# Optimization experiments

Measured on AMD Instinct MI355X. Metric: run time of the kernel, lower is better.

The kernel has to match this reference:

```python
import jax, jax.numpy as jnp
import numpy as np

T = 8192        # timesteps
IN = 512        # input_size
H = 1024        # hidden_layer_size
OUT = 256       # output_size
STEP = 0.25     # ODE solver step_size
NSUB = 4        # euler substeps per unit time interval (t spacing = 1)


def setup_inputs() -> dict:
    key = jax.random.key(0)
    ks = jax.random.split(key, 16)
    def lin(k, out_d, in_d):
        kw, kb = jax.random.split(k)
        W = jax.random.normal(kw, (out_d, in_d), jnp.float32) / np.sqrt(in_d).astype(np.float32)
        b = jax.random.normal(kb, (out_d, 1), jnp.float32) * 0.01
        return W, b
    W_in, b_in = lin(ks[0], H, IN)      # linear_in
    W_h, b_h = lin(ks[1], H, H)         # linear_hidden
    W_h2, b_h2 = lin(ks[2], H, H)       # linear_hidden2
    W_f1, b_f1 = lin(ks[3], H, H)       # ode_func.linear
    W_f2, b_f2 = lin(ks[4], H, H)       # ode_func.linear2
    W_dec, b_dec = lin(ks[5], OUT, H)   # decoder
    x = jax.random.normal(ks[6], (T, IN, 1), jnp.float32)
    t = jnp.arange(T, dtype=jnp.float32)
    return dict(t=t, x=x, W_in=W_in, b_in=b_in, W_h=W_h, b_h=b_h,
                W_h2=W_h2, b_h2=b_h2, W_f1=W_f1, b_f1=b_f1,
                W_f2=W_f2, b_f2=b_f2, W_dec=W_dec, b_dec=b_dec)


def reference(t, x, W_in, b_in, W_h, b_h, W_h2, b_h2, W_f1, b_f1, W_f2, b_f2, W_dec, b_dec):
    # ODE_Func: f(h) = W_f2 @ tanh(W_f1 @ h + b_f1) + b_f2   (autonomous; t unused)
    def ode_f(h):
        return W_f2 @ jnp.tanh(W_f1 @ h + b_f1) + b_f2

    dts = (t[1:] - t[:-1]) / NSUB  # (T-1,) euler substep sizes (fixed-grid euler)

    def step(h, inp):
        x_i, dt = inp
        # odeint(ode_func, h, t[i-1:i+1], method='euler', step_size=STEP)
        for _ in range(NSUB):
            h = h + dt * ode_f(h)
        # RNN cell update
        pre = W_in @ x_i + b_in + W_h @ h + b_h          # (H,1)
        h_new = jnp.tanh(W_h2 @ jnp.tanh(pre) + b_h2)    # (H,1)
        return h_new, None

    h0 = jnp.zeros((W_h.shape[0], 1), x.dtype)
    # original loop skips i == 0 entirely (h stays zeros there)
    h_T, _ = jax.lax.scan(step, h0, (x[1:], dts))
    return W_dec @ h_T + b_dec  # (OUT, 1)
```

## Files before the change

kernel.cpp:

```cpp
#include <hip/hip_runtime.h>
#include <math.h>


#define TSTEPS 8192
#define INP    512
#define HDIM   1024
#define OUTD   256
#define NWG    64
#define BLK    256

typedef unsigned long long u64;
typedef unsigned int u32;

__device__ __forceinline__ u64 aload(u64* p) {
    return __hip_atomic_load(p, __ATOMIC_RELAXED, __HIP_MEMORY_SCOPE_AGENT);
}
__device__ __forceinline__ void astore(u64* p, u64 v) {
    __hip_atomic_store(p, v, __ATOMIC_RELAXED, __HIP_MEMORY_SCOPE_AGENT);
}
__device__ __forceinline__ u64 pack(u32 tag, float f) {
    return ((u64)tag << 32) | (u64)__float_as_uint(f);
}

__global__ __launch_bounds__(256)
void mm1024(const float* __restrict__ A, const float* __restrict__ B,
            float* __restrict__ C) {
    __shared__ float As[64][17];
    __shared__ float Bs[16][65];
    const int tid = threadIdx.x;
    const int tx = tid & 15, ty = tid >> 4;
    const int r0 = blockIdx.y * 64, c0 = blockIdx.x * 64;
    float acc[4][4] = {};
    for (int k0 = 0; k0 < HDIM; k0 += 16) {
        const int ar = tid >> 2, ac = (tid & 3) * 4;
        const float4 av = *reinterpret_cast<const float4*>(
            A + (size_t)(r0 + ar) * HDIM + k0 + ac);
        As[ar][ac] = av.x; As[ar][ac + 1] = av.y;
        As[ar][ac + 2] = av.z; As[ar][ac + 3] = av.w;
        const int br = tid >> 4, bc = (tid & 15) * 4;
        const float4 bv = *reinterpret_cast<const float4*>(
            B + (size_t)(k0 + br) * HDIM + c0 + bc);
        Bs[br][bc] = bv.x; Bs[br][bc + 1] = bv.y;
        Bs[br][bc + 2] = bv.z; Bs[br][bc + 3] = bv.w;
        __syncthreads();
        #pragma unroll
        for (int kk = 0; kk < 16; ++kk) {
            float a[4], b[4];
            #pragma unroll
            for (int i2 = 0; i2 < 4; ++i2) a[i2] = As[ty * 4 + i2][kk];
            #pragma unroll
            for (int j2 = 0; j2 < 4; ++j2) b[j2] = Bs[kk][tx * 4 + j2];
            #pragma unroll
            for (int i2 = 0; i2 < 4; ++i2)
                #pragma unroll
                for (int j2 = 0; j2 < 4; ++j2)
                    acc[i2][j2] = fmaf(a[i2], b[j2], acc[i2][j2]);
        }
        __syncthreads();
    }
    #pragma unroll
    for (int i2 = 0; i2 < 4; ++i2)
        #pragma unroll
        for (int j2 = 0; j2 < 4; ++j2)
            C[(size_t)(r0 + ty * 4 + i2) * HDIM + c0 + tx * 4 + j2] = acc[i2][j2];
}

__global__ __launch_bounds__(BLK, 1)
void ode_rnn_persistent(
    const float* __restrict__ t,    const float* __restrict__ x,
    const float* __restrict__ W_in, const float* __restrict__ b_in,
    const float* __restrict__ W_h,  const float* __restrict__ b_h,
    const float* __restrict__ W_h2, const float* __restrict__ b_h2,
    const float* __restrict__ W_f1, const float* __restrict__ b_f1,
    const float* __restrict__ b_f2,
    const float* __restrict__ W_dec, const float* __restrict__ b_dec,
    const float* __restrict__ Mw,   const float* __restrict__ Pw,
    float* __restrict__ out,
    u64* QA, u64* QB, u64* QC, u64* QD)
{
    __shared__ __align__(16) float lds[HDIM];
    const int tid = threadIdx.x;
    const int wg  = blockIdx.x;
    const int seg = tid & 15;
    const int row = wg * 16 + (tid >> 4);

    auto stage = [&](u64* q, u32 tag) {
        __syncthreads();
        const int i0 = tid, i1 = tid + 256, i2 = tid + 512, i3 = tid + 768;
        u64 v0, v1, v2, v3;
        for (;;) {
            v0 = aload(q + i0); v1 = aload(q + i1);
            v2 = aload(q + i2); v3 = aload(q + i3);
            const bool ok = ((u32)(v0 >> 32) == tag) & ((u32)(v1 >> 32) == tag) &
                            ((u32)(v2 >> 32) == tag) & ((u32)(v3 >> 32) == tag);
            if (ok) break;
        }
        lds[i0] = __uint_as_float((u32)v0); lds[i1] = __uint_as_float((u32)v1);
        lds[i2] = __uint_as_float((u32)v2); lds[i3] = __uint_as_float((u32)v3);
        __syncthreads();
    };

    auto pref16 = [&](float4* w, const float* Wbase) {
        const float4* p = reinterpret_cast<const float4*>(Wbase + (size_t)row * HDIM);
        #pragma unroll
        for (int j = 0; j < 16; ++j) w[j] = p[j * 16 + seg];
    };
    auto dot16 = [&](const float4* w) {
        float a = 0.f;
        #pragma unroll
        for (int j = 0; j < 16; ++j) {
            const float4 v = *reinterpret_cast<const float4*>(lds + j * 64 + seg * 4);
            a = fmaf(w[j].x, v.x, a); a = fmaf(w[j].y, v.y, a);
            a = fmaf(w[j].z, v.z, a); a = fmaf(w[j].w, v.w, a);
        }
        return a;
    };
    auto reduce16 = [&](float a) {
        #pragma unroll
        for (int off = 8; off; off >>= 1) a += __shfl_down(a, off, 16);
        return a;
    };

    const float bf1_r = b_f1[row];
    const float bih_r = b_in[row] + b_h[row];
    const float bh2_r = b_h2[row];

    float c1_own, c2_own;
    {
        #pragma unroll
        for (int k = 0; k < 4; ++k) lds[tid + k * 256] = b_f2[tid + k * 256];
        __syncthreads();
        float4 w[16];
        pref16(w, W_f1); c1_own = reduce16(dot16(w));
        pref16(w, W_h);  c2_own = reduce16(dot16(w));
    }

    float z_own = bf1_r;
    float y_own = 0.f;
    u32 eA = 0, eB = 0, eC = 0, eD = 0;
    float4 wa[16], wb[16];

    #pragma unroll 1
    for (int i = 1; i < TSTEPS; ++i) {
        const float dt = (t[i] - t[i - 1]) * 0.25f;

        ++eA;
        if (seg == 0) astore(&QA[row], pack(eA, tanhf(z_own)));
        float4 xr[8], wir[8];
        {
            const float4* xp = reinterpret_cast<const float4*>(x + (size_t)i * INP);
            const float4* wp = reinterpret_cast<const float4*>(W_in + (size_t)row * INP);
            #pragma unroll
            for (int j = 0; j < 8; ++j) { xr[j] = xp[j * 16 + seg]; wir[j] = wp[j * 16 + seg]; }
        }
        pref16(wa, Mw); pref16(wb, Pw);
        stage(QA, eA);
        float winx;
        {
            float a_ = 0.f;
            #pragma unroll
            for (int j = 0; j < 8; ++j) {
                a_ = fmaf(wir[j].x, xr[j].x, a_); a_ = fmaf(wir[j].y, xr[j].y, a_);
                a_ = fmaf(wir[j].z, xr[j].z, a_); a_ = fmaf(wir[j].w, xr[j].w, a_);
            }
            winx = reduce16(a_);
        }
        {
            const float md = reduce16(dot16(wa));
            const float pd = reduce16(dot16(wb));
            if (seg == 0) { z_own = fmaf(dt, md + c1_own, z_own);
                            y_own = fmaf(dt, pd + c2_own, y_own); }
        }

        ++eB;
        if (seg == 0) astore(&QB[row], pack(eB, tanhf(z_own)));
        pref16(wa, Mw); pref16(wb, Pw);
        stage(QB, eB);
        {
            const float md = reduce16(dot16(wa));
            const float pd = reduce16(dot16(wb));
            if (seg == 0) { z_own = fmaf(dt, md + c1_own, z_own);
                            y_own = fmaf(dt, pd + c2_own, y_own); }
        }

        ++eA;
        if (seg == 0) astore(&QA[row], pack(eA, tanhf(z_own)));
        pref16(wa, Mw); pref16(wb, Pw);
        stage(QA, eA);
        {
            const float md = reduce16(dot16(wa));
            const float pd = reduce16(dot16(wb));
            if (seg == 0) { z_own = fmaf(dt, md + c1_own, z_own);
                            y_own = fmaf(dt, pd + c2_own, y_own); }
        }

        ++eB;
        if (seg == 0) astore(&QB[row], pack(eB, tanhf(z_own)));
        pref16(wb, Pw);
        stage(QB, eB);
        float a_val = 0.f;
        {
            const float pd = reduce16(dot16(wb));
            if (seg == 0) {
                const float y4 = fmaf(dt, pd + c2_own, y_own);
                a_val = tanhf(y4 + winx + bih_r);
            }
        }

        ++eC;
        if (seg == 0) astore(&QC[row], pack(eC, a_val));
        pref16(wa, W_h2);
        stage(QC, eC);
        float h_new = 0.f;
        {
            const float hd = reduce16(dot16(wa));
            if (seg == 0) h_new = tanhf(hd + bh2_r);
        }

        ++eD;
        if (seg == 0) astore(&QD[row], pack(eD, h_new));
        pref16(wa, W_f1);
        stage(QD, eD);
        {
            const float zd = reduce16(dot16(wa));
            pref16(wb, W_h);
            const float yd = reduce16(dot16(wb));
            if (seg == 0) { z_own = zd + bf1_r; y_own = yd; }
        }
    }

    {
        const int rl = tid >> 6, s2 = tid & 63;
        const int orow = wg * 4 + rl;
        const float4* wd = reinterpret_cast<const float4*>(W_dec + (size_t)orow * HDIM);
        float acc = 0.f;
        #pragma unroll
        for (int j = 0; j < 4; ++j) {
            const float4 w = wd[j * 64 + s2];
            const float4 v = *reinterpret_cast<const float4*>(lds + j * 256 + s2 * 4);
            acc = fmaf(w.x, v.x, acc); acc = fmaf(w.y, v.y, acc);
            acc = fmaf(w.z, v.z, acc); acc = fmaf(w.w, v.w, acc);
        }
        #pragma unroll
        for (int off = 32; off; off >>= 1) acc += __shfl_down(acc, off, 64);
        if (s2 == 0) out[orow] = acc + b_dec[orow];
    }
}

extern "C" void kernel_launch(void* const* d_in, const int* in_sizes, int n_in,
                              void* d_out, int out_size, void* d_ws, size_t ws_size,
                              hipStream_t stream) {
    const float* t     = (const float*)d_in[0];
    const float* x     = (const float*)d_in[1];
    const float* W_in  = (const float*)d_in[2];
    const float* b_in  = (const float*)d_in[3];
    const float* W_h   = (const float*)d_in[4];
    const float* b_h   = (const float*)d_in[5];
    const float* W_h2  = (const float*)d_in[6];
    const float* b_h2  = (const float*)d_in[7];
    const float* W_f1  = (const float*)d_in[8];
    const float* b_f1  = (const float*)d_in[9];
    const float* W_f2  = (const float*)d_in[10];
    const float* b_f2  = (const float*)d_in[11];
    const float* W_dec = (const float*)d_in[12];
    const float* b_dec = (const float*)d_in[13];
    float* out = (float*)d_out;

    unsigned char* ws = (unsigned char*)d_ws;
    float* Mw = (float*)(ws);
    float* Pw = (float*)(ws + (size_t)4 * 1024 * 1024);
    u64*   QA = (u64*)(ws + (size_t)8 * 1024 * 1024);
    u64*   QB = QA + HDIM;
    u64*   QC = QB + HDIM;
    u64*   QD = QC + HDIM;

    mm1024<<<dim3(16, 16), 256, 0, stream>>>(W_f1, W_f2, Mw);
    mm1024<<<dim3(16, 16), 256, 0, stream>>>(W_h,  W_f2, Pw);

    hipMemsetAsync(ws + (size_t)8 * 1024 * 1024, 0, 4 * HDIM * sizeof(u64), stream);

    ode_rnn_persistent<<<dim3(NWG), dim3(BLK), 0, stream>>>(
        t, x, W_in, b_in, W_h, b_h, W_h2, b_h2, W_f1, b_f1, b_f2,
        W_dec, b_dec, Mw, Pw, out, QA, QB, QC, QD);
}
```

Baseline: 100.5 ms.

## Restructure persistent ODE-RNN to 256 single-wave blocks with register-resident weights

Splits the persistent kernel from 64 blocks of 256 threads into 256 single-wavefront blocks that each own 4 hidden rows. The M and P operator rows and the W_in rows are now kept in registers for the whole run instead of being reloaded every substep. Each wave polls the flag-tagged exchange queues directly into registers and uses wave-wide shuffle reductions, which removes the LDS staging and __syncthreads barriers. The cost is much higher register pressure and more blocks spinning on the global queues at every stage.

After: 123.5 ms. 22.9% more time.

```diff
diff --git a/kernel.cpp b/kernel.cpp
--- a/kernel.cpp
+++ b/kernel.cpp
@@ -6,8 +6,8 @@
 #define INP    512
 #define HDIM   1024
 #define OUTD   256
-#define NWG    64
-#define BLK    256
+#define NWG    256
+#define BLK    64
 
 typedef unsigned long long u64;
 typedef unsigned int u32;
@@ -78,172 +78,210 @@
     float* __restrict__ out,
     u64* QA, u64* QB, u64* QC, u64* QD)
 {
-    __shared__ __align__(16) float lds[HDIM];
-    const int tid = threadIdx.x;
-    const int wg  = blockIdx.x;
-    const int seg = tid & 15;
-    const int row = wg * 16 + (tid >> 4);
-
-    auto stage = [&](u64* q, u32 tag) {
-        __syncthreads();
-        const int i0 = tid, i1 = tid + 256, i2 = tid + 512, i3 = tid + 768;
-        u64 v0, v1, v2, v3;
+    const int lane = threadIdx.x;
+    const int gw   = blockIdx.x;
+    const int r0   = gw * 4;
+
+    auto bflyAll = [&](float& a) {
+        #pragma unroll
+        for (int off = 32; off; off >>= 1) a += __shfl_xor(a, off);
+    };
+    auto sel4 = [&](const float (&a)[4]) {
+        float s = a[0];
+        s = (lane == 1) ? a[1] : s;
+        s = (lane == 2) ? a[2] : s;
+        s = (lane == 3) ? a[3] : s;
+        return s;
+    };
+    auto pubTanh = [&](u64* q, u32 e, float pre) {
+        if (lane < 4) astore(&q[r0 + lane], pack(e, tanhf(pre)));
+    };
+    auto waitq = [&](u64* q, u32 tag, u64 (&v)[16]) {
         for (;;) {
-            v0 = aload(q + i0); v1 = aload(q + i1);
-            v2 = aload(q + i2); v3 = aload(q + i3);
-            const bool ok = ((u32)(v0 >> 32) == tag) & ((u32)(v1 >> 32) == tag) &
-                            ((u32)(v2 >> 32) == tag) & ((u32)(v3 >> 32) == tag);
-            if (ok) break;
-        }
-        lds[i0] = __uint_as_float((u32)v0); lds[i1] = __uint_as_float((u32)v1);
-        lds[i2] = __uint_as_float((u32)v2); lds[i3] = __uint_as_float((u32)v3);
-        __syncthreads();
-    };
-
-    auto pref16 = [&](float4* w, const float* Wbase) {
-        const float4* p = reinterpret_cast<const float4*>(Wbase + (size_t)row * HDIM);
-        #pragma unroll
-        for (int j = 0; j < 16; ++j) w[j] = p[j * 16 + seg];
-    };
-    auto dot16 = [&](const float4* w) {
-        float a = 0.f;
+            #pragma unroll
+            for (int j = 0; j < 16; ++j) v[j] = aload(q + j * 64 + lane);
+            bool ok = true;
+            #pragma unroll
+            for (int j = 0; j < 16; ++j) ok &= ((u32)(v[j] >> 32) == tag);
+            if (__all(ok)) break;
+        }
+    };
+    auto loadRows16 = [&](const float* __restrict__ W, float (&w)[4][16]) {
+        #pragma unroll
+        for (int r = 0; r < 4; ++r)
+            #pragma unroll
+            for (int j = 0; j < 16; ++j)
+                w[r][j] = W[(size_t)(r0 + r) * HDIM + j * 64 + lane];
+    };
+    auto dotDual = [&](const float (&wa)[4][16], const float (&wb)[4][16],
+                       const u64 (&v)[16], float (&oa)[4], float (&ob)[4]) {
+        float aa[4] = {}, ab[4] = {};
         #pragma unroll
         for (int j = 0; j < 16; ++j) {
-            const float4 v = *reinterpret_cast<const float4*>(lds + j * 64 + seg * 4);
-            a = fmaf(w[j].x, v.x, a); a = fmaf(w[j].y, v.y, a);
-            a = fmaf(w[j].z, v.z, a); a = fmaf(w[j].w, v.w, a);
-        }
-        return a;
-    };
-    auto reduce16 = [&](float a) {
-        #pragma unroll
-        for (int off = 8; off; off >>= 1) a += __shfl_down(a, off, 16);
-        return a;
-    };
-
-    const float bf1_r = b_f1[row];
-    const float bih_r = b_in[row] + b_h[row];
-    const float bh2_r = b_h2[row];
-
-    float c1_own, c2_own;
+            const float uv = __uint_as_float((u32)v[j]);
+            #pragma unroll
+            for (int r = 0; r < 4; ++r) {
+                aa[r] = fmaf(wa[r][j], uv, aa[r]);
+                ab[r] = fmaf(wb[r][j], uv, ab[r]);
+            }
+        }
+        #pragma unroll
+        for (int off = 32; off; off >>= 1)
+            #pragma unroll
+            for (int r = 0; r < 4; ++r) {
+                aa[r] += __shfl_xor(aa[r], off);
+                ab[r] += __shfl_xor(ab[r], off);
+            }
+        #pragma unroll
+        for (int r = 0; r < 4; ++r) { oa[r] = aa[r]; ob[r] = ab[r]; }
+    };
+    auto dotOne = [&](const float (&wa)[4][16], const u64 (&v)[16],
+                      float (&oa)[4]) {
+        float aa[4] = {};
+        #pragma unroll
+        for (int j = 0; j < 16; ++j) {
+            const float uv = __uint_as_float((u32)v[j]);
+            #pragma unroll
+            for (int r = 0; r < 4; ++r) aa[r] = fmaf(wa[r][j], uv, aa[r]);
+        }
+        #pragma unroll
+        for (int off = 32; off; off >>= 1)
+            #pragma unroll
+            for (int r = 0; r < 4; ++r) aa[r] += __shfl_xor(aa[r], off);
+        #pragma unroll
+        for (int r = 0; r < 4; ++r) oa[r] = aa[r];
+    };
+
+    float m[4][16], p[4][16];
+    loadRows16(Mw, m);
+    loadRows16(Pw, p);
+    float wir[4][8];
+    #pragma unroll
+    for (int r = 0; r < 4; ++r)
+        #pragma unroll
+        for (int j = 0; j < 8; ++j)
+            wir[r][j] = W_in[(size_t)(r0 + r) * INP + j * 64 + lane];
+
+    float bf1r[4], bihr[4], bh2r[4];
+    #pragma unroll
+    for (int r = 0; r < 4; ++r) {
+        bf1r[r] = b_f1[r0 + r];
+        bihr[r] = b_in[r0 + r] + b_h[r0 + r];
+        bh2r[r] = b_h2[r0 + r];
+    }
+
+    float c1[4], c2[4];
     {
-        #pragma unroll
-        for (int k = 0; k < 4; ++k) lds[tid + k * 256] = b_f2[tid + k * 256];
-        __syncthreads();
-        float4 w[16];
-        pref16(w, W_f1); c1_own = reduce16(dot16(w));
-        pref16(w, W_h);  c2_own = reduce16(dot16(w));
-    }
-
-    float z_own = bf1_r;
-    float y_own = 0.f;
+        float bv[16];
+        #pragma unroll
+        for (int j = 0; j < 16; ++j) bv[j] = b_f2[j * 64 + lane];
+        float wt[4][16];
+        loadRows16(W_f1, wt);
+        #pragma unroll
+        for (int r = 0; r < 4; ++r) {
+            float a = 0.f;
+            #pragma unroll
+            for (int j = 0; j < 16; ++j) a = fmaf(wt[r][j], bv[j], a);
+            bflyAll(a); c1[r] = a;
+        }
+        loadRows16(W_h, wt);
+        #pragma unroll
+        for (int r = 0; r < 4; ++r) {
+            float a = 0.f;
+            #pragma unroll
+            for (int j = 0; j < 16; ++j) a = fmaf(wt[r][j], bv[j], a);
+            bflyAll(a); c2[r] = a;
+        }
+    }
+
+    float z[4], y[4];
+    #pragma unroll
+    for (int r = 0; r < 4; ++r) { z[r] = bf1r[r]; y[r] = 0.f; }
+
     u32 eA = 0, eB = 0, eC = 0, eD = 0;
-    float4 wa[16], wb[16];
+    u64 v[16];
+    float xr[8];
+    float wbufA[4][16], wbufB[4][16];
+
+    auto odeSub = [&](u64* q, u32 e, float dt) {
+        pubTanh(q, e, sel4(z));
+        waitq(q, e, v);
+        float md[4], pd[4];
+        dotDual(m, p, v, md, pd);
+        #pragma unroll
+        for (int r = 0; r < 4; ++r) {
+            z[r] = fmaf(dt, md[r] + c1[r], z[r]);
+            y[r] = fmaf(dt, pd[r] + c2[r], y[r]);
+        }
+    };
 
     #pragma unroll 1
     for (int i = 1; i < TSTEPS; ++i) {
         const float dt = (t[i] - t[i - 1]) * 0.25f;
-
-        ++eA;
-        if (seg == 0) astore(&QA[row], pack(eA, tanhf(z_own)));
-        float4 xr[8], wir[8];
+        const float* xrow = x + (size_t)i * INP;
+
+        odeSub(QA, ++eA, dt);
+        #pragma unroll
+        for (int j = 0; j < 8; ++j) xr[j] = xrow[j * 64 + lane];
+        odeSub(QB, ++eB, dt);
+        odeSub(QA, ++eA, dt);
+
+        ++eB;
+        pubTanh(QB, eB, sel4(z));
+        float winx[4];
         {
-            const float4* xp = reinterpret_cast<const float4*>(x + (size_t)i * INP);
-            const float4* wp = reinterpret_cast<const float4*>(W_in + (size_t)row * INP);
-            #pragma unroll
-            for (int j = 0; j < 8; ++j) { xr[j] = xp[j * 16 + seg]; wir[j] = wp[j * 16 + seg]; }
-        }
-        pref16(wa, Mw); pref16(wb, Pw);
-        stage(QA, eA);
-        float winx;
-        {
-            float a_ = 0.f;
-            #pragma unroll
-            for (int j = 0; j < 8; ++j) {
-                a_ = fmaf(wir[j].x, xr[j].x, a_); a_ = fmaf(wir[j].y, xr[j].y, a_);
-                a_ = fmaf(wir[j].z, xr[j].z, a_); a_ = fmaf(wir[j].w, xr[j].w, a_);
-            }
-            winx = reduce16(a_);
-        }
-        {
-            const float md = reduce16(dot16(wa));
-            const float pd = reduce16(dot16(wb));
-            if (seg == 0) { z_own = fmaf(dt, md + c1_own, z_own);
-                            y_own = fmaf(dt, pd + c2_own, y_own); }
-        }
-
-        ++eB;
-        if (seg == 0) astore(&QB[row], pack(eB, tanhf(z_own)));
-        pref16(wa, Mw); pref16(wb, Pw);
-        stage(QB, eB);
-        {
-            const float md = reduce16(dot16(wa));
-            const float pd = reduce16(dot16(wb));
-            if (seg == 0) { z_own = fmaf(dt, md + c1_own, z_own);
-                            y_own = fmaf(dt, pd + c2_own, y_own); }
-        }
-
-        ++eA;
-        if (seg == 0) astore(&QA[row], pack(eA, tanhf(z_own)));
-        pref16(wa, Mw); pref16(wb, Pw);
-        stage(QA, eA);
-        {
-            const float md = reduce16(dot16(wa));
-            const float pd = reduce16(dot16(wb));
-            if (seg == 0) { z_own = fmaf(dt, md + c1_own, z_own);
-                            y_own = fmaf(dt, pd + c2_own, y_own); }
-        }
-
-        ++eB;
-        if (seg == 0) astore(&QB[row], pack(eB, tanhf(z_own)));
-        pref16(wb, Pw);
-        stage(QB, eB);
-        float a_val = 0.f;
-        {
-            const float pd = reduce16(dot16(wb));
-            if (seg == 0) {
-                const float y4 = fmaf(dt, pd + c2_own, y_own);
-                a_val = tanhf(y4 + winx + bih_r);
-            }
-        }
+            float aw[4] = {};
+            #pragma unroll
+            for (int j = 0; j < 8; ++j)
+                #pragma unroll
+                for (int r = 0; r < 4; ++r)
+                    aw[r] = fmaf(wir[r][j], xr[j], aw[r]);
+            #pragma unroll
+            for (int off = 32; off; off >>= 1)
+                #pragma unroll
+                for (int r = 0; r < 4; ++r) aw[r] += __shfl_xor(aw[r], off);
+            #pragma unroll
+            for (int r = 0; r < 4; ++r) winx[r] = aw[r];
+        }
+        waitq(QB, eB, v);
+        float pd[4];
+        dotOne(p, v, pd);
+        float apre[4];
+        #pragma unroll
+        for (int r = 0; r < 4; ++r)
+            apre[r] = fmaf(dt, pd[r] + c2[r], y[r]) + winx[r] + bihr[r];
 
         ++eC;
-        if (seg == 0) astore(&QC[row], pack(eC, a_val));
-        pref16(wa, W_h2);
-        stage(QC, eC);
-        float h_new = 0.f;
-        {
-            const float hd = reduce16(dot16(wa));
-            if (seg == 0) h_new = tanhf(hd + bh2_r);
-        }
+        pubTanh(QC, eC, sel4(apre));
+        loadRows16(W_h2, wbufA);
+        waitq(QC, eC, v);
+        float hd[4];
+        dotOne(wbufA, v, hd);
+        float hpre[4];
+        #pragma unroll
+        for (int r = 0; r < 4; ++r) hpre[r] = hd[r] + bh2r[r];
 
         ++eD;
-        if (seg == 0) astore(&QD[row], pack(eD, h_new));
-        pref16(wa, W_f1);
-        stage(QD, eD);
-        {
-            const float zd = reduce16(dot16(wa));
-            pref16(wb, W_h);
-            const float yd = reduce16(dot16(wb));
-            if (seg == 0) { z_own = zd + bf1_r; y_own = yd; }
-        }
-    }
-
+        pubTanh(QD, eD, sel4(hpre));
+        loadRows16(W_f1, wbufA);
+        loadRows16(W_h, wbufB);
+        waitq(QD, eD, v);
+        float zd[4], yd[4];
+        dotDual(wbufA, wbufB, v, zd, yd);
+        #pragma unroll
+        for (int r = 0; r < 4; ++r) { z[r] = zd[r] + bf1r[r]; y[r] = yd[r]; }
+    }
+
+    waitq(QD, eD, v);
     {
-        const int rl = tid >> 6, s2 = tid & 63;
-        const int orow = wg * 4 + rl;
-        const float4* wd = reinterpret_cast<const float4*>(W_dec + (size_t)orow * HDIM);
         float acc = 0.f;
         #pragma unroll
-        for (int j = 0; j < 4; ++j) {
-            const float4 w = wd[j * 64 + s2];
-            const float4 v = *reinterpret_cast<const float4*>(lds + j * 256 + s2 * 4);
-            acc = fmaf(w.x, v.x, acc); acc = fmaf(w.y, v.y, acc);
-            acc = fmaf(w.z, v.z, acc); acc = fmaf(w.w, v.w, acc);
-        }
-        #pragma unroll
-        for (int off = 32; off; off >>= 1) acc += __shfl_down(acc, off, 64);
-        if (s2 == 0) out[orow] = acc + b_dec[orow];
+        for (int j = 0; j < 16; ++j) {
+            const float w = W_dec[(size_t)gw * HDIM + j * 64 + lane];
+            acc = fmaf(w, __uint_as_float((u32)v[j]), acc);
+        }
+        bflyAll(acc);
+        if (lane == 0) out[gw] = acc + b_dec[gw];
     }
 }
 
```

## Keep Mw/Pw/W_in rows register-resident and replicate exchange queues across WGs

Applied to the files above, without the earlier changes.

Mw, Pw and W_in rows are now loaded into registers once before the time loop instead of being refetched from memory at every Euler substep. The inter-workgroup exchange buffers are replicated eight times; each workgroup publishes to all replicas and polls the one chosen by its block index, which spreads out the polling traffic. Tanh is moved from the producer into publish, dot products are fused in pairs sharing the LDS reads, and W_h2/W_f1/W_h loads are reordered to overlap with waits. This raises register pressure to roughly 80 float4 per thread and multiplies the publish stores by eight.

New measurement: 105.3 ms. 1.05x slower.

```diff
diff --git a/kernel.cpp b/kernel.cpp
--- a/kernel.cpp
+++ b/kernel.cpp
@@ -8,6 +8,7 @@
 #define OUTD   256
 #define NWG    64
 #define BLK    256
+#define NREP   8
 
 typedef unsigned long long u64;
 typedef unsigned int u32;
@@ -83,14 +84,20 @@
     const int wg  = blockIdx.x;
     const int seg = tid & 15;
     const int row = wg * 16 + (tid >> 4);
+    const int rep = wg & (NREP - 1);
+
+    auto publish = [&](u64* q, u32 e, float pre) {
+        if (seg < 8) astore(q + (size_t)seg * HDIM + row, pack(e, tanhf(pre)));
+    };
 
     auto stage = [&](u64* q, u32 tag) {
+        u64* base = q + (size_t)rep * HDIM;
         __syncthreads();
         const int i0 = tid, i1 = tid + 256, i2 = tid + 512, i3 = tid + 768;
         u64 v0, v1, v2, v3;
         for (;;) {
-            v0 = aload(q + i0); v1 = aload(q + i1);
-            v2 = aload(q + i2); v3 = aload(q + i3);
+            v0 = aload(base + i0); v1 = aload(base + i1);
+            v2 = aload(base + i2); v3 = aload(base + i3);
             const bool ok = ((u32)(v0 >> 32) == tag) & ((u32)(v1 >> 32) == tag) &
                             ((u32)(v2 >> 32) == tag) & ((u32)(v3 >> 32) == tag);
             if (ok) break;
@@ -100,12 +107,17 @@
         __syncthreads();
     };
 
-    auto pref16 = [&](float4* w, const float* Wbase) {
-        const float4* p = reinterpret_cast<const float4*>(Wbase + (size_t)row * HDIM);
-        #pragma unroll
-        for (int j = 0; j < 16; ++j) w[j] = p[j * 16 + seg];
-    };
-    auto dot16 = [&](const float4* w) {
+    auto pref16 = [&](const float* W, float4 (&w)[16]) {
+        const float4* pW = reinterpret_cast<const float4*>(W + (size_t)row * HDIM);
+        #pragma unroll
+        for (int j = 0; j < 16; ++j) w[j] = pW[j * 16 + seg];
+    };
+    auto red16 = [&](float a) {
+        #pragma unroll
+        for (int off = 8; off; off >>= 1) a += __shfl_xor(a, off, 16);
+        return a;
+    };
+    auto dotLds = [&](const float4 (&w)[16]) {
         float a = 0.f;
         #pragma unroll
         for (int j = 0; j < 16; ++j) {
@@ -113,119 +125,121 @@
             a = fmaf(w[j].x, v.x, a); a = fmaf(w[j].y, v.y, a);
             a = fmaf(w[j].z, v.z, a); a = fmaf(w[j].w, v.w, a);
         }
-        return a;
-    };
-    auto reduce16 = [&](float a) {
-        #pragma unroll
-        for (int off = 8; off; off >>= 1) a += __shfl_down(a, off, 16);
-        return a;
-    };
+        return red16(a);
+    };
+    auto dotLds2 = [&](const float4 (&wa)[16], const float4 (&wb)[16],
+                       float& oa, float& ob) {
+        float a = 0.f, b = 0.f;
+        #pragma unroll
+        for (int j = 0; j < 16; ++j) {
+            const float4 v = *reinterpret_cast<const float4*>(lds + j * 64 + seg * 4);
+            a = fmaf(wa[j].x, v.x, a); a = fmaf(wa[j].y, v.y, a);
+            a = fmaf(wa[j].z, v.z, a); a = fmaf(wa[j].w, v.w, a);
+            b = fmaf(wb[j].x, v.x, b); b = fmaf(wb[j].y, v.y, b);
+            b = fmaf(wb[j].z, v.z, b); b = fmaf(wb[j].w, v.w, b);
+        }
+        oa = red16(a); ob = red16(b);
+    };
+
+    float4 m16[16], p16[16], wir[8];
+    pref16(Mw, m16);
+    pref16(Pw, p16);
+    {
+        const float4* pW = reinterpret_cast<const float4*>(W_in + (size_t)row * INP);
+        #pragma unroll
+        for (int j = 0; j < 8; ++j) wir[j] = pW[j * 16 + seg];
+    }
 
     const float bf1_r = b_f1[row];
     const float bih_r = b_in[row] + b_h[row];
     const float bh2_r = b_h2[row];
 
+    float4 wbufA[16], wbufB[16];
+
     float c1_own, c2_own;
     {
         #pragma unroll
         for (int k = 0; k < 4; ++k) lds[tid + k * 256] = b_f2[tid + k * 256];
         __syncthreads();
-        float4 w[16];
-        pref16(w, W_f1); c1_own = reduce16(dot16(w));
-        pref16(w, W_h);  c2_own = reduce16(dot16(w));
+        pref16(W_f1, wbufA); c1_own = dotLds(wbufA);
+        pref16(W_h,  wbufA); c2_own = dotLds(wbufA);
     }
 
     float z_own = bf1_r;
     float y_own = 0.f;
     u32 eA = 0, eB = 0, eC = 0, eD = 0;
-    float4 wa[16], wb[16];
+    float4 xr[8];
 
     #pragma unroll 1
     for (int i = 1; i < TSTEPS; ++i) {
         const float dt = (t[i] - t[i - 1]) * 0.25f;
 
         ++eA;
-        if (seg == 0) astore(&QA[row], pack(eA, tanhf(z_own)));
-        float4 xr[8], wir[8];
+        publish(QA, eA, z_own);
+        stage(QA, eA);
         {
             const float4* xp = reinterpret_cast<const float4*>(x + (size_t)i * INP);
-            const float4* wp = reinterpret_cast<const float4*>(W_in + (size_t)row * INP);
-            #pragma unroll
-            for (int j = 0; j < 8; ++j) { xr[j] = xp[j * 16 + seg]; wir[j] = wp[j * 16 + seg]; }
-        }
-        pref16(wa, Mw); pref16(wb, Pw);
+            #pragma unroll
+            for (int j = 0; j < 8; ++j) xr[j] = xp[j * 16 + seg];
+        }
+        {
+            float md, pd; dotLds2(m16, p16, md, pd);
+            z_own = fmaf(dt, md + c1_own, z_own);
+            y_own = fmaf(dt, pd + c2_own, y_own);
+        }
+
+        ++eB;
+        publish(QB, eB, z_own);
+        stage(QB, eB);
+        {
+            float md, pd; dotLds2(m16, p16, md, pd);
+            z_own = fmaf(dt, md + c1_own, z_own);
+            y_own = fmaf(dt, pd + c2_own, y_own);
+        }
+
+        ++eA;
+        publish(QA, eA, z_own);
         stage(QA, eA);
+        {
+            float md, pd; dotLds2(m16, p16, md, pd);
+            z_own = fmaf(dt, md + c1_own, z_own);
+            y_own = fmaf(dt, pd + c2_own, y_own);
+        }
+
+        ++eB;
+        publish(QB, eB, z_own);
         float winx;
         {
-            float a_ = 0.f;
+            float a = 0.f;
             #pragma unroll
             for (int j = 0; j < 8; ++j) {
-                a_ = fmaf(wir[j].x, xr[j].x, a_); a_ = fmaf(wir[j].y, xr[j].y, a_);
-                a_ = fmaf(wir[j].z, xr[j].z, a_); a_ = fmaf(wir[j].w, xr[j].w, a_);
+                a = fmaf(wir[j].x, xr[j].x, a); a = fmaf(wir[j].y, xr[j].y, a);
+                a = fmaf(wir[j].z, xr[j].z, a); a = fmaf(wir[j].w, xr[j].w, a);
             }
-            winx = reduce16(a_);
-        }
-        {
-            const float md = reduce16(dot16(wa));
-            const float pd = reduce16(dot16(wb));
-            if (seg == 0) { z_own = fmaf(dt, md + c1_own, z_own);
-                            y_own = fmaf(dt, pd + c2_own, y_own); }
-        }
-
-        ++eB;
-        if (seg == 0) astore(&QB[row], pack(eB, tanhf(z_own)));
-        pref16(wa, Mw); pref16(wb, Pw);
+            winx = red16(a);
+        }
         stage(QB, eB);
-        {
-            const float md = reduce16(dot16(wa));
-            const float pd = reduce16(dot16(wb));
-            if (seg == 0) { z_own = fmaf(dt, md + c1_own, z_own);
-                            y_own = fmaf(dt, pd + c2_own, y_own); }
-        }
-
-        ++eA;
-        if (seg == 0) astore(&QA[row], pack(eA, tanhf(z_own)));
-        pref16(wa, Mw); pref16(wb, Pw);
-        stage(QA, eA);
-        {
-            const float md = reduce16(dot16(wa));
-            const float pd = reduce16(dot16(wb));
-            if (seg == 0) { z_own = fmaf(dt, md + c1_own, z_own);
-                            y_own = fmaf(dt, pd + c2_own, y_own); }
-        }
-
-        ++eB;
-        if (seg == 0) astore(&QB[row], pack(eB, tanhf(z_own)));
-        pref16(wb, Pw);
-        stage(QB, eB);
-        float a_val = 0.f;
-        {
-            const float pd = reduce16(dot16(wb));
-            if (seg == 0) {
-                const float y4 = fmaf(dt, pd + c2_own, y_own);
-                a_val = tanhf(y4 + winx + bih_r);
-            }
+        pref16(W_h2, wbufA);
+        float apre;
+        {
+            const float pd = dotLds(p16);
+            apre = fmaf(dt, pd + c2_own, y_own) + winx + bih_r;
         }
 
         ++eC;
-        if (seg == 0) astore(&QC[row], pack(eC, a_val));
-        pref16(wa, W_h2);
+        publish(QC, eC, apre);
         stage(QC, eC);
-        float h_new = 0.f;
-        {
-            const float hd = reduce16(dot16(wa));
-            if (seg == 0) h_new = tanhf(hd + bh2_r);
-        }
+        pref16(W_f1, wbufB);
+        const float hpre = dotLds(wbufA) + bh2_r;
 
         ++eD;
-        if (seg == 0) astore(&QD[row], pack(eD, h_new));
-        pref16(wa, W_f1);
+        publish(QD, eD, hpre);
+        pref16(W_h, wbufA);
         stage(QD, eD);
         {
-            const float zd = reduce16(dot16(wa));
-            pref16(wb, W_h);
-            const float yd = reduce16(dot16(wb));
-            if (seg == 0) { z_own = zd + bf1_r; y_own = yd; }
+            float zd, yd; dotLds2(wbufB, wbufA, zd, yd);
+            z_own = zd + bf1_r;
+            y_own = yd;
         }
     }
 
@@ -270,14 +284,15 @@
     float* Mw = (float*)(ws);
     float* Pw = (float*)(ws + (size_t)4 * 1024 * 1024);
     u64*   QA = (u64*)(ws + (size_t)8 * 1024 * 1024);
-    u64*   QB = QA + HDIM;
-    u64*   QC = QB + HDIM;
-    u64*   QD = QC + HDIM;
+    u64*   QB = QA + (size_t)NREP * HDIM;
+    u64*   QC = QB + (size_t)NREP * HDIM;
+    u64*   QD = QC + (size_t)NREP * HDIM;
 
     mm1024<<<dim3(16, 16), 256, 0, stream>>>(W_f1, W_f2, Mw);
     mm1024<<<dim3(16, 16), 256, 0, stream>>>(W_h,  W_f2, Pw);
 
-    hipMemsetAsync(ws + (size_t)8 * 1024 * 1024, 0, 4 * HDIM * sizeof(u64), stream);
+    hipMemsetAsync(ws + (size_t)8 * 1024 * 1024, 0,
+                   (size_t)4 * NREP * HDIM * sizeof(u64), stream);
 
     ode_rnn_persistent<<<dim3(NWG), dim3(BLK), 0, stream>>>(
         t, x, W_in, b_in, W_h, b_h, W_h2, b_h2, W_f1, b_f1, b_f2,
```
